# Kernel optimization log

Hardware: AMD Instinct MI355X
Metric: run time of the kernel (lower is better)

## Reference

```python
import jax, jax.numpy as jnp
import numpy as np

B = 16384
D = 128
N_LAYER = 2
USER_NUM, ITEM_NUM, ENTITY_NUM = 100000, 50000, 50000
H1, H2 = 256, 128  # hidden_layers


def setup_inputs() -> dict:
    key = jax.random.key(0)
    ks = jax.random.split(key, 20)
    inp = {
        'user_ids': jax.random.randint(ks[0], (B,), 0, USER_NUM),
        'item_ids': jax.random.randint(ks[1], (B,), 0, ITEM_NUM),
        'rec_target': jax.random.uniform(ks[2], (B,), dtype=jnp.float32),
        # embedding tables
        'user_tbl': jax.random.normal(ks[3], (USER_NUM, D), dtype=jnp.float32) * 0.02,
        'item_tbl': jax.random.normal(ks[4], (ITEM_NUM, D), dtype=jnp.float32) * 0.02,
        'entity_tbl': jax.random.normal(ks[5], (ENTITY_NUM, D), dtype=jnp.float32) * 0.02,
        # cross-compress weights (torch.rand -> uniform)
        'w_vv': jax.random.uniform(ks[6], (D, 1), dtype=jnp.float32),
        'w_ev': jax.random.uniform(ks[7], (D, 1), dtype=jnp.float32),
        'w_ve': jax.random.uniform(ks[8], (D, 1), dtype=jnp.float32),
        'w_ee': jax.random.uniform(ks[9], (D, 1), dtype=jnp.float32),
        'bias_v': jax.random.uniform(ks[10], (1,), dtype=jnp.float32),
        'bias_e': jax.random.uniform(ks[11], (1,), dtype=jnp.float32),
        # user low MLP (Linear D->D)
        'Wu': jax.random.normal(ks[12], (D, D), dtype=jnp.float32) * 0.05,
        'bu': jnp.zeros((D,), dtype=jnp.float32),
        # rec MLP: 2D -> H1 -> H2 -> 1
        'W1': jax.random.normal(ks[13], (2 * D, H1), dtype=jnp.float32) * 0.05,
        'b1': jnp.zeros((H1,), dtype=jnp.float32),
        'W2': jax.random.normal(ks[14], (H1, H2), dtype=jnp.float32) * 0.05,
        'b2': jnp.zeros((H2,), dtype=jnp.float32),
        'W3': jax.random.normal(ks[15], (H2, 1), dtype=jnp.float32) * 0.05,
        'b3': jnp.zeros((1,), dtype=jnp.float32),
    }
    return inp


def _cross_compress(item, head, w_vv, w_ev, w_ve, w_ee, bias_v, bias_e):
    # c[b,i,j] = item[b,i]*head[b,j]; c_t[b,i,j] = head[b,i]*item[b,j]
    # (c @ w)[b,i] = item[b,i] * (head @ w)[b]; (c_t @ w)[b,i] = head[b,i] * (item @ w)[b]
    hv = head @ w_vv  # [B,1]
    iv = item @ w_ev  # [B,1]
    he = head @ w_ve  # [B,1]
    ie = item @ w_ee  # [B,1]
    item_c = item * hv + head * iv + bias_v
    head_c = item * he + head * ie + bias_e
    return item_c, head_c


def reference(user_ids, item_ids, rec_target, user_tbl, item_tbl, entity_tbl,
              w_vv, w_ev, w_ve, w_ee, bias_v, bias_e,
              Wu, bu, W1, b1, W2, b2, W3, b3):
    # train_type == 'rec' branch
    user_embed = user_tbl[user_ids]      # [B, D]
    item_embed = item_tbl[item_ids]      # [B, D]
    head_embed = entity_tbl[item_ids]    # [B, D]
    for _ in range(N_LAYER):
        user_embed = jax.nn.relu(user_embed @ Wu + bu)  # linear_layer (dropout=identity at eval)
        item_embed, head_embed = _cross_compress(
            item_embed, head_embed, w_vv, w_ev, w_ve, w_ee, bias_v, bias_e)
    high = jnp.concatenate([user_embed, item_embed], axis=1)  # [B, 2D]
    h = jax.nn.relu(high @ W1 + b1)
    h = jax.nn.relu(h @ W2 + b2)
    rec_out = jax.nn.relu(h @ W3 + b3)  # [B, 1]
    return rec_out[:, 0], rec_target
```

## Files before the change

### kernel.cpp

```cpp
#include <hip/hip_runtime.h>

#define BATCH 16384
#define DIM 128

typedef __attribute__((ext_vector_type(8))) short short8;
typedef __attribute__((ext_vector_type(4))) float floatx4;

__device__ __forceinline__ ushort f2bf(float f) {
    union { float f; uint u; } c; c.f = f;
    return (ushort)((c.u + 0x7FFFu + ((c.u >> 16) & 1u)) >> 16);
}
__device__ __forceinline__ float bf2f(ushort h) {
    union { uint u; float f; } c; c.u = ((uint)h) << 16;
    return c.f;
}
__device__ __forceinline__ ushort4 f4_to_bf4(float4 v) {
    return make_ushort4(f2bf(v.x), f2bf(v.y), f2bf(v.z), f2bf(v.w));
}

__device__ __forceinline__ int slot_idx(int KT, int m, int k) {
    return (((m >> 4) * KT + (k >> 5)) << 6) + (((k >> 3) & 3) << 4) + (m & 15);
}

__global__ __launch_bounds__(256) void convert_kernel(
    const float* __restrict__ Wu, const float* __restrict__ W1,
    const float* __restrict__ W2, short8* __restrict__ WF)
{
    const int f    = blockIdx.x * 4 + (threadIdx.x >> 6);
    const int lane = threadIdx.x & 63;
    const int q = lane >> 4, r = lane & 15;
    const float* W; int N, nt, kf, fl; short8* dst;
    if (f < 32)       { W = Wu; N = 128; fl = f;       nt = fl >> 2; kf = fl & 3; dst = WF;         }
    else if (f < 160) { W = W1; N = 256; fl = f - 32;  nt = fl >> 3; kf = fl & 7; dst = WF + 2048;  }
    else              { W = W2; N = 128; fl = f - 160; nt = fl >> 3; kf = fl & 7; dst = WF + 10240; }
    const int n = nt * 16 + r, k0 = kf * 32 + q * 8;
    short8 v;
    #pragma unroll
    for (int j = 0; j < 8; ++j)
        v[j] = (short)f2bf(W[(size_t)(k0 + j) * N + n]);
    dst[fl * 64 + lane] = v;
}

template<int KF, int NT, int DKT>
__device__ __forceinline__ void layer_mfma(
    const short8* __restrict__ src, const short8* __restrict__ WF,
    const float* __restrict__ bias, ushort* __restrict__ dst, int tid)
{
    const int wave = tid >> 6, lane = tid & 63;
    const int q = lane >> 4, r = lane & 15;
    short8 a[2][KF];
    #pragma unroll
    for (int mt = 0; mt < 2; ++mt)
        #pragma unroll
        for (int kf = 0; kf < KF; ++kf)
            a[mt][kf] = src[(mt * KF + kf) * 64 + lane];
    #pragma unroll
    for (int nt = wave; nt < NT; nt += 4) {
        const int col = nt * 16 + r;
        short8 b[KF];
        #pragma unroll
        for (int kf = 0; kf < KF; ++kf)
            b[kf] = WF[(nt * KF + kf) * 64 + lane];
        const float bs = bias[col];
        const int kc = col >> 5, qc = (col >> 3) & 3, e = col & 7;
        #pragma unroll
        for (int mt = 0; mt < 2; ++mt) {
            floatx4 acc = {0.f, 0.f, 0.f, 0.f};
            #pragma unroll
            for (int kf = 0; kf < KF; ++kf)
                acc = __builtin_amdgcn_mfma_f32_16x16x32_bf16(a[mt][kf], b[kf], acc, 0, 0, 0);
            #pragma unroll
            for (int rr = 0; rr < 4; ++rr) {
                const int rlow = q * 4 + rr;
                dst[(size_t)((((mt * DKT + kc) << 6) + (qc << 4) + rlow) * 8 + e)] =
                    f2bf(fmaxf(acc[rr] + bs, 0.f));
            }
        }
    }
}

__global__ __launch_bounds__(256) void fused_kernel(
    const int* __restrict__ user_ids, const int* __restrict__ item_ids,
    const float* __restrict__ rec_target,
    const float* __restrict__ user_tbl, const float* __restrict__ item_tbl,
    const float* __restrict__ entity_tbl,
    const float* __restrict__ w_vv, const float* __restrict__ w_ev,
    const float* __restrict__ w_ve, const float* __restrict__ w_ee,
    const float* __restrict__ bias_v, const float* __restrict__ bias_e,
    const short8* __restrict__ WF, const float* __restrict__ bu,
    const float* __restrict__ b1, const float* __restrict__ b2,
    const float* __restrict__ W3, const float* __restrict__ b3,
    float* __restrict__ out)
{
    __shared__ short8 sU0[512];
    __shared__ short8 sU1[512];
    __shared__ short8 sHI[1024];
    __shared__ short8 sH1[1024];
    __shared__ short8 sH2[512];

    const int r0   = blockIdx.x * 32;
    const int tid  = threadIdx.x;
    const int wave = tid >> 6, lane = tid & 63;
    const int q    = lane >> 4, r = lane & 15;
    const int row  = tid >> 3, l = tid & 7;

    short8 bw[2][4];
    #pragma unroll
    for (int i = 0; i < 2; ++i) {
        const int nt = wave + i * 4;
        #pragma unroll
        for (int kf = 0; kf < 4; ++kf)
            bw[i][kf] = WF[(nt * 4 + kf) * 64 + lane];
    }

    if (tid < 32) out[BATCH + r0 + tid] = rec_target[r0 + tid];

    {
        const int uid = user_ids[r0 + row];
        const float4* src = (const float4*)(user_tbl + (size_t)uid * DIM + l * 16);
        ushort* p = (ushort*)sU0;
        #pragma unroll
        for (int i = 0; i < 4; ++i) {
            const int col = l * 16 + i * 4;
            *(ushort4*)&p[slot_idx(4, row, col) * 8 + (col & 7)] = f4_to_bf4(src[i]);
        }
    }

    {
        const int id = item_ids[r0 + row];
        const float4* ip = (const float4*)(item_tbl   + (size_t)id * DIM + l * 16);
        const float4* hp = (const float4*)(entity_tbl + (size_t)id * DIM + l * 16);
        float4 it4[4], hd4[4];
        #pragma unroll
        for (int i = 0; i < 4; ++i) { it4[i] = ip[i]; hd4[i] = hp[i]; }
        const float bv = bias_v[0], be = bias_e[0];
        #pragma unroll
        for (int lay = 0; lay < 2; ++lay) {
            float hv = 0.f, iv = 0.f, he = 0.f, ie = 0.f;
            #pragma unroll
            for (int i = 0; i < 4; ++i) {
                float4 wvv = ((const float4*)w_vv)[l * 4 + i];
                float4 wev = ((const float4*)w_ev)[l * 4 + i];
                float4 wve = ((const float4*)w_ve)[l * 4 + i];
                float4 wee = ((const float4*)w_ee)[l * 4 + i];
                hv += hd4[i].x * wvv.x + hd4[i].y * wvv.y + hd4[i].z * wvv.z + hd4[i].w * wvv.w;
                iv += it4[i].x * wev.x + it4[i].y * wev.y + it4[i].z * wev.z + it4[i].w * wev.w;
                he += hd4[i].x * wve.x + hd4[i].y * wve.y + hd4[i].z * wve.z + hd4[i].w * wve.w;
                ie += it4[i].x * wee.x + it4[i].y * wee.y + it4[i].z * wee.z + it4[i].w * wee.w;
            }
            hv += __shfl_xor(hv, 1); hv += __shfl_xor(hv, 2); hv += __shfl_xor(hv, 4);
            iv += __shfl_xor(iv, 1); iv += __shfl_xor(iv, 2); iv += __shfl_xor(iv, 4);
            he += __shfl_xor(he, 1); he += __shfl_xor(he, 2); he += __shfl_xor(he, 4);
            ie += __shfl_xor(ie, 1); ie += __shfl_xor(ie, 2); ie += __shfl_xor(ie, 4);
            #pragma unroll
            for (int i = 0; i < 4; ++i) {
                float4 t = it4[i], h = hd4[i];
                it4[i].x = t.x * hv + h.x * iv + bv;  hd4[i].x = t.x * he + h.x * ie + be;
                it4[i].y = t.y * hv + h.y * iv + bv;  hd4[i].y = t.y * he + h.y * ie + be;
                it4[i].z = t.z * hv + h.z * iv + bv;  hd4[i].z = t.z * he + h.z * ie + be;
                it4[i].w = t.w * hv + h.w * iv + bv;  hd4[i].w = t.w * he + h.w * ie + be;
            }
        }
        ushort* p = (ushort*)sHI;
        #pragma unroll
        for (int i = 0; i < 4; ++i) {
            const int col = 128 + l * 16 + i * 4;
            *(ushort4*)&p[slot_idx(8, row, col) * 8 + (col & 7)] = f4_to_bf4(it4[i]);
        }
    }
    __syncthreads();

    {
        short8 a[2][4];
        #pragma unroll
        for (int mt = 0; mt < 2; ++mt)
            #pragma unroll
            for (int kf = 0; kf < 4; ++kf)
                a[mt][kf] = sU0[(mt * 4 + kf) * 64 + lane];
        #pragma unroll
        for (int i = 0; i < 2; ++i) {
            const int col = (wave + i * 4) * 16 + r;
            const float bs = bu[col];
            const int kc = col >> 5, qc = (col >> 3) & 3, e = col & 7;
            #pragma unroll
            for (int mt = 0; mt < 2; ++mt) {
                floatx4 acc = {0.f, 0.f, 0.f, 0.f};
                #pragma unroll
                for (int kf = 0; kf < 4; ++kf)
                    acc = __builtin_amdgcn_mfma_f32_16x16x32_bf16(a[mt][kf], bw[i][kf], acc, 0, 0, 0);
                ushort* dst = (ushort*)sU1;
                #pragma unroll
                for (int rr = 0; rr < 4; ++rr)
                    dst[(((mt * 4 + kc) << 6) + (qc << 4) + q * 4 + rr) * 8 + e] =
                        f2bf(fmaxf(acc[rr] + bs, 0.f));
            }
        }
    }
    __syncthreads();

    {
        short8 a[2][4];
        #pragma unroll
        for (int mt = 0; mt < 2; ++mt)
            #pragma unroll
            for (int kf = 0; kf < 4; ++kf)
                a[mt][kf] = sU1[(mt * 4 + kf) * 64 + lane];
        #pragma unroll
        for (int i = 0; i < 2; ++i) {
            const int col = (wave + i * 4) * 16 + r;
            const float bs = bu[col];
            const int kc = col >> 5, qc = (col >> 3) & 3, e = col & 7;
            #pragma unroll
            for (int mt = 0; mt < 2; ++mt) {
                floatx4 acc = {0.f, 0.f, 0.f, 0.f};
                #pragma unroll
                for (int kf = 0; kf < 4; ++kf)
                    acc = __builtin_amdgcn_mfma_f32_16x16x32_bf16(a[mt][kf], bw[i][kf], acc, 0, 0, 0);
                ushort* dst = (ushort*)sHI;
                #pragma unroll
                for (int rr = 0; rr < 4; ++rr)
                    dst[(((mt * 8 + kc) << 6) + (qc << 4) + q * 4 + rr) * 8 + e] =
                        f2bf(fmaxf(acc[rr] + bs, 0.f));
            }
        }
    }
    __syncthreads();

    layer_mfma<8, 16, 8>(sHI, WF + 2048,  b1, (ushort*)sH1, tid);
    __syncthreads();
    layer_mfma<8, 8, 4>(sH1, WF + 10240,  b2, (ushort*)sH2, tid);
    __syncthreads();

    {
        float p = 0.f;
        #pragma unroll
        for (int i = 0; i < 2; ++i) {
            const int c8 = l * 2 + i;
            short8 h = sH2[(((row >> 4) * 4 + (c8 >> 2)) << 6) + ((c8 & 3) << 4) + (row & 15)];
            float4 w0 = ((const float4*)W3)[c8 * 2];
            float4 w1 = ((const float4*)W3)[c8 * 2 + 1];
            p += bf2f((ushort)h[0]) * w0.x + bf2f((ushort)h[1]) * w0.y
               + bf2f((ushort)h[2]) * w0.z + bf2f((ushort)h[3]) * w0.w
               + bf2f((ushort)h[4]) * w1.x + bf2f((ushort)h[5]) * w1.y
               + bf2f((ushort)h[6]) * w1.z + bf2f((ushort)h[7]) * w1.w;
        }
        p += __shfl_xor(p, 1); p += __shfl_xor(p, 2); p += __shfl_xor(p, 4);
        if (l == 0) out[r0 + row] = fmaxf(p + b3[0], 0.f);
    }
}

extern "C" void kernel_launch(void* const* d_in, const int* in_sizes, int n_in,
                              void* d_out, int out_size, void* d_ws, size_t ws_size,
                              hipStream_t stream)
{
    const int*   user_ids   = (const int*)  d_in[0];
    const int*   item_ids   = (const int*)  d_in[1];
    const float* rec_target = (const float*)d_in[2];
    const float* user_tbl   = (const float*)d_in[3];
    const float* item_tbl   = (const float*)d_in[4];
    const float* entity_tbl = (const float*)d_in[5];
    const float* w_vv       = (const float*)d_in[6];
    const float* w_ev       = (const float*)d_in[7];
    const float* w_ve       = (const float*)d_in[8];
    const float* w_ee       = (const float*)d_in[9];
    const float* bias_v     = (const float*)d_in[10];
    const float* bias_e     = (const float*)d_in[11];
    const float* Wu         = (const float*)d_in[12];
    const float* bu         = (const float*)d_in[13];
    const float* W1         = (const float*)d_in[14];
    const float* b1         = (const float*)d_in[15];
    const float* W2         = (const float*)d_in[16];
    const float* b2         = (const float*)d_in[17];
    const float* W3         = (const float*)d_in[18];
    const float* b3         = (const float*)d_in[19];
    float* out = (float*)d_out;

    short8* WF = (short8*)d_ws;

    convert_kernel<<<56, 256, 0, stream>>>(Wu, W1, W2, WF);
    fused_kernel<<<BATCH / 32, 256, 0, stream>>>(
        user_ids, item_ids, rec_target, user_tbl, item_tbl, entity_tbl,
        w_vv, w_ev, w_ve, w_ee, bias_v, bias_e,
        WF, bu, b1, b2, W3, b3, out);
}
```

Baseline: 155.6 us.

## Use 512-thread blocks, hoist gathers, fuse final W3 dot into layer-2 epilogue

The fused kernel now runs 8 waves per 32-row block instead of 4, so each wave owns one output column tile in the 128-wide layers and two in the 256-wide layer. All three embedding gathers are issued up front, and the cross-compress math now runs while the first user MLP layer is computed. The final H2->1 projection is folded into the second MLP layer's epilogue using shuffle reductions and a small shared partial-sum array, which removes the sH2 buffer and one LDS round trip. In exchange, each wave reloads the A fragments per m-tile, and the larger blocks may change occupancy and register pressure.

```diff
diff --git a/kernel.cpp b/kernel.cpp
--- a/kernel.cpp
+++ b/kernel.cpp
@@ -9,13 +9,6 @@
 __device__ __forceinline__ ushort f2bf(float f) {
     union { float f; uint u; } c; c.f = f;
     return (ushort)((c.u + 0x7FFFu + ((c.u >> 16) & 1u)) >> 16);
-}
-__device__ __forceinline__ float bf2f(ushort h) {
-    union { uint u; float f; } c; c.u = ((uint)h) << 16;
-    return c.f;
-}
-__device__ __forceinline__ ushort4 f4_to_bf4(float4 v) {
-    return make_ushort4(f2bf(v.x), f2bf(v.y), f2bf(v.z), f2bf(v.w));
 }
 
 __device__ __forceinline__ int slot_idx(int KT, int m, int k) {
@@ -41,45 +34,7 @@
     dst[fl * 64 + lane] = v;
 }
 
-template<int KF, int NT, int DKT>
-__device__ __forceinline__ void layer_mfma(
-    const short8* __restrict__ src, const short8* __restrict__ WF,
-    const float* __restrict__ bias, ushort* __restrict__ dst, int tid)
-{
-    const int wave = tid >> 6, lane = tid & 63;
-    const int q = lane >> 4, r = lane & 15;
-    short8 a[2][KF];
-    #pragma unroll
-    for (int mt = 0; mt < 2; ++mt)
-        #pragma unroll
-        for (int kf = 0; kf < KF; ++kf)
-            a[mt][kf] = src[(mt * KF + kf) * 64 + lane];
-    #pragma unroll
-    for (int nt = wave; nt < NT; nt += 4) {
-        const int col = nt * 16 + r;
-        short8 b[KF];
-        #pragma unroll
-        for (int kf = 0; kf < KF; ++kf)
-            b[kf] = WF[(nt * KF + kf) * 64 + lane];
-        const float bs = bias[col];
-        const int kc = col >> 5, qc = (col >> 3) & 3, e = col & 7;
-        #pragma unroll
-        for (int mt = 0; mt < 2; ++mt) {
-            floatx4 acc = {0.f, 0.f, 0.f, 0.f};
-            #pragma unroll
-            for (int kf = 0; kf < KF; ++kf)
-                acc = __builtin_amdgcn_mfma_f32_16x16x32_bf16(a[mt][kf], b[kf], acc, 0, 0, 0);
-            #pragma unroll
-            for (int rr = 0; rr < 4; ++rr) {
-                const int rlow = q * 4 + rr;
-                dst[(size_t)((((mt * DKT + kc) << 6) + (qc << 4) + rlow) * 8 + e)] =
-                    f2bf(fmaxf(acc[rr] + bs, 0.f));
-            }
-        }
-    }
-}
-
-__global__ __launch_bounds__(256) void fused_kernel(
+__global__ __launch_bounds__(512) void fused_kernel(
     const int* __restrict__ user_ids, const int* __restrict__ item_ids,
     const float* __restrict__ rec_target,
     const float* __restrict__ user_tbl, const float* __restrict__ item_tbl,
@@ -96,64 +51,84 @@
     __shared__ short8 sU1[512];
     __shared__ short8 sHI[1024];
     __shared__ short8 sH1[1024];
-    __shared__ short8 sH2[512];
+    __shared__ float  sP[8][32];
 
     const int r0   = blockIdx.x * 32;
     const int tid  = threadIdx.x;
     const int wave = tid >> 6, lane = tid & 63;
     const int q    = lane >> 4, r = lane & 15;
-    const int row  = tid >> 3, l = tid & 7;
-
-    short8 bw[2][4];
+    const int row  = tid >> 4, l = tid & 15;
+
+    const int uid = user_ids[r0 + row];
+    const int iid = item_ids[r0 + row];
+    const float4* up = (const float4*)(user_tbl   + (size_t)uid * DIM + l * 8);
+    const float4* ip = (const float4*)(item_tbl   + (size_t)iid * DIM + l * 8);
+    const float4* hp = (const float4*)(entity_tbl + (size_t)iid * DIM + l * 8);
+    float4 us4[2] = { up[0], up[1] };
+    float4 it4[2] = { ip[0], ip[1] };
+    float4 hd4[2] = { hp[0], hp[1] };
+
+    short8 bw[4];
     #pragma unroll
-    for (int i = 0; i < 2; ++i) {
-        const int nt = wave + i * 4;
-        #pragma unroll
-        for (int kf = 0; kf < 4; ++kf)
-            bw[i][kf] = WF[(nt * 4 + kf) * 64 + lane];
-    }
+    for (int kf = 0; kf < 4; ++kf)
+        bw[kf] = WF[(wave * 4 + kf) * 64 + lane];
 
     if (tid < 32) out[BATCH + r0 + tid] = rec_target[r0 + tid];
 
     {
-        const int uid = user_ids[r0 + row];
-        const float4* src = (const float4*)(user_tbl + (size_t)uid * DIM + l * 16);
-        ushort* p = (ushort*)sU0;
-        #pragma unroll
-        for (int i = 0; i < 4; ++i) {
-            const int col = l * 16 + i * 4;
-            *(ushort4*)&p[slot_idx(4, row, col) * 8 + (col & 7)] = f4_to_bf4(src[i]);
-        }
-    }
-
-    {
-        const int id = item_ids[r0 + row];
-        const float4* ip = (const float4*)(item_tbl   + (size_t)id * DIM + l * 16);
-        const float4* hp = (const float4*)(entity_tbl + (size_t)id * DIM + l * 16);
-        float4 it4[4], hd4[4];
-        #pragma unroll
-        for (int i = 0; i < 4; ++i) { it4[i] = ip[i]; hd4[i] = hp[i]; }
+        const float* uf = (const float*)us4;
+        short8 v;
+        #pragma unroll
+        for (int j = 0; j < 8; ++j) v[j] = (short)f2bf(uf[j]);
+        sU0[slot_idx(4, row, l * 8)] = v;
+    }
+    __syncthreads();
+
+    {
+        short8 a[2][4];
+        #pragma unroll
+        for (int mt = 0; mt < 2; ++mt)
+            #pragma unroll
+            for (int kf = 0; kf < 4; ++kf)
+                a[mt][kf] = sU0[(mt * 4 + kf) * 64 + lane];
+        const int col = wave * 16 + r;
+        const float bs = bu[col];
+        const int kc = col >> 5, qc = (col >> 3) & 3, e = col & 7;
+        ushort* dst = (ushort*)sU1;
+        #pragma unroll
+        for (int mt = 0; mt < 2; ++mt) {
+            floatx4 acc = {0.f, 0.f, 0.f, 0.f};
+            #pragma unroll
+            for (int kf = 0; kf < 4; ++kf)
+                acc = __builtin_amdgcn_mfma_f32_16x16x32_bf16(a[mt][kf], bw[kf], acc, 0, 0, 0);
+            #pragma unroll
+            for (int rr = 0; rr < 4; ++rr)
+                dst[(((mt * 4 + kc) << 6) + (qc << 4) + q * 4 + rr) * 8 + e] =
+                    f2bf(fmaxf(acc[rr] + bs, 0.f));
+        }
+    }
+    {
         const float bv = bias_v[0], be = bias_e[0];
         #pragma unroll
         for (int lay = 0; lay < 2; ++lay) {
             float hv = 0.f, iv = 0.f, he = 0.f, ie = 0.f;
             #pragma unroll
-            for (int i = 0; i < 4; ++i) {
-                float4 wvv = ((const float4*)w_vv)[l * 4 + i];
-                float4 wev = ((const float4*)w_ev)[l * 4 + i];
-                float4 wve = ((const float4*)w_ve)[l * 4 + i];
-                float4 wee = ((const float4*)w_ee)[l * 4 + i];
+            for (int i = 0; i < 2; ++i) {
+                float4 wvv = ((const float4*)w_vv)[l * 2 + i];
+                float4 wev = ((const float4*)w_ev)[l * 2 + i];
+                float4 wve = ((const float4*)w_ve)[l * 2 + i];
+                float4 wee = ((const float4*)w_ee)[l * 2 + i];
                 hv += hd4[i].x * wvv.x + hd4[i].y * wvv.y + hd4[i].z * wvv.z + hd4[i].w * wvv.w;
                 iv += it4[i].x * wev.x + it4[i].y * wev.y + it4[i].z * wev.z + it4[i].w * wev.w;
                 he += hd4[i].x * wve.x + hd4[i].y * wve.y + hd4[i].z * wve.z + hd4[i].w * wve.w;
                 ie += it4[i].x * wee.x + it4[i].y * wee.y + it4[i].z * wee.z + it4[i].w * wee.w;
             }
-            hv += __shfl_xor(hv, 1); hv += __shfl_xor(hv, 2); hv += __shfl_xor(hv, 4);
-            iv += __shfl_xor(iv, 1); iv += __shfl_xor(iv, 2); iv += __shfl_xor(iv, 4);
-            he += __shfl_xor(he, 1); he += __shfl_xor(he, 2); he += __shfl_xor(he, 4);
-            ie += __shfl_xor(ie, 1); ie += __shfl_xor(ie, 2); ie += __shfl_xor(ie, 4);
-            #pragma unroll
-            for (int i = 0; i < 4; ++i) {
+            hv += __shfl_xor(hv, 1); hv += __shfl_xor(hv, 2); hv += __shfl_xor(hv, 4); hv += __shfl_xor(hv, 8);
+            iv += __shfl_xor(iv, 1); iv += __shfl_xor(iv, 2); iv += __shfl_xor(iv, 4); iv += __shfl_xor(iv, 8);
+            he += __shfl_xor(he, 1); he += __shfl_xor(he, 2); he += __shfl_xor(he, 4); he += __shfl_xor(he, 8);
+            ie += __shfl_xor(ie, 1); ie += __shfl_xor(ie, 2); ie += __shfl_xor(ie, 4); ie += __shfl_xor(ie, 8);
+            #pragma unroll
+            for (int i = 0; i < 2; ++i) {
                 float4 t = it4[i], h = hd4[i];
                 it4[i].x = t.x * hv + h.x * iv + bv;  hd4[i].x = t.x * he + h.x * ie + be;
                 it4[i].y = t.y * hv + h.y * iv + bv;  hd4[i].y = t.y * he + h.y * ie + be;
@@ -161,12 +136,11 @@
                 it4[i].w = t.w * hv + h.w * iv + bv;  hd4[i].w = t.w * he + h.w * ie + be;
             }
         }
-        ushort* p = (ushort*)sHI;
-        #pragma unroll
-        for (int i = 0; i < 4; ++i) {
-            const int col = 128 + l * 16 + i * 4;
-            *(ushort4*)&p[slot_idx(8, row, col) * 8 + (col & 7)] = f4_to_bf4(it4[i]);
-        }
+        const float* itf = (const float*)it4;
+        short8 v;
+        #pragma unroll
+        for (int j = 0; j < 8; ++j) v[j] = (short)f2bf(itf[j]);
+        sHI[slot_idx(8, row, 128 + l * 8)] = v;
     }
     __syncthreads();
 
@@ -176,47 +150,48 @@
         for (int mt = 0; mt < 2; ++mt)
             #pragma unroll
             for (int kf = 0; kf < 4; ++kf)
-                a[mt][kf] = sU0[(mt * 4 + kf) * 64 + lane];
-        #pragma unroll
-        for (int i = 0; i < 2; ++i) {
-            const int col = (wave + i * 4) * 16 + r;
-            const float bs = bu[col];
-            const int kc = col >> 5, qc = (col >> 3) & 3, e = col & 7;
-            #pragma unroll
-            for (int mt = 0; mt < 2; ++mt) {
+                a[mt][kf] = sU1[(mt * 4 + kf) * 64 + lane];
+        const int col = wave * 16 + r;
+        const float bs = bu[col];
+        const int kc = col >> 5, qc = (col >> 3) & 3, e = col & 7;
+        ushort* dst = (ushort*)sHI;
+        #pragma unroll
+        for (int mt = 0; mt < 2; ++mt) {
+            floatx4 acc = {0.f, 0.f, 0.f, 0.f};
+            #pragma unroll
+            for (int kf = 0; kf < 4; ++kf)
+                acc = __builtin_amdgcn_mfma_f32_16x16x32_bf16(a[mt][kf], bw[kf], acc, 0, 0, 0);
+            #pragma unroll
+            for (int rr = 0; rr < 4; ++rr)
+                dst[(((mt * 8 + kc) << 6) + (qc << 4) + q * 4 + rr) * 8 + e] =
+                    f2bf(fmaxf(acc[rr] + bs, 0.f));
+        }
+    }
+    __syncthreads();
+
+    {
+        const short8* WF1 = WF + 2048;
+        ushort* dst = (ushort*)sH1;
+        #pragma unroll
+        for (int mt = 0; mt < 2; ++mt) {
+            short8 a[8];
+            #pragma unroll
+            for (int kf = 0; kf < 8; ++kf)
+                a[kf] = sHI[(mt * 8 + kf) * 64 + lane];
+            #pragma unroll
+            for (int i = 0; i < 2; ++i) {
+                const int nt = wave + i * 8;
+                short8 b[8];
+                #pragma unroll
+                for (int kf = 0; kf < 8; ++kf)
+                    b[kf] = WF1[(nt * 8 + kf) * 64 + lane];
+                const int col = nt * 16 + r;
+                const float bs = b1[col];
+                const int kc = col >> 5, qc = (col >> 3) & 3, e = col & 7;
                 floatx4 acc = {0.f, 0.f, 0.f, 0.f};
                 #pragma unroll
-                for (int kf = 0; kf < 4; ++kf)
-                    acc = __builtin_amdgcn_mfma_f32_16x16x32_bf16(a[mt][kf], bw[i][kf], acc, 0, 0, 0);
-                ushort* dst = (ushort*)sU1;
-                #pragma unroll
-                for (int rr = 0; rr < 4; ++rr)
-                    dst[(((mt * 4 + kc) << 6) + (qc << 4) + q * 4 + rr) * 8 + e] =
-                        f2bf(fmaxf(acc[rr] + bs, 0.f));
-            }
-        }
-    }
-    __syncthreads();
-
-    {
-        short8 a[2][4];
-        #pragma unroll
-        for (int mt = 0; mt < 2; ++mt)
-            #pragma unroll
-            for (int kf = 0; kf < 4; ++kf)
-                a[mt][kf] = sU1[(mt * 4 + kf) * 64 + lane];
-        #pragma unroll
-        for (int i = 0; i < 2; ++i) {
-            const int col = (wave + i * 4) * 16 + r;
-            const float bs = bu[col];
-            const int kc = col >> 5, qc = (col >> 3) & 3, e = col & 7;
-            #pragma unroll
-            for (int mt = 0; mt < 2; ++mt) {
-                floatx4 acc = {0.f, 0.f, 0.f, 0.f};
-                #pragma unroll
-                for (int kf = 0; kf < 4; ++kf)
-                    acc = __builtin_amdgcn_mfma_f32_16x16x32_bf16(a[mt][kf], bw[i][kf], acc, 0, 0, 0);
-                ushort* dst = (ushort*)sHI;
+                for (int kf = 0; kf < 8; ++kf)
+                    acc = __builtin_amdgcn_mfma_f32_16x16x32_bf16(a[kf], b[kf], acc, 0, 0, 0);
                 #pragma unroll
                 for (int rr = 0; rr < 4; ++rr)
                     dst[(((mt * 8 + kc) << 6) + (qc << 4) + q * 4 + rr) * 8 + e] =
@@ -226,26 +201,54 @@
     }
     __syncthreads();
 
-    layer_mfma<8, 16, 8>(sHI, WF + 2048,  b1, (ushort*)sH1, tid);
-    __syncthreads();
-    layer_mfma<8, 8, 4>(sH1, WF + 10240,  b2, (ushort*)sH2, tid);
-    __syncthreads();
-
-    {
+    {
+        const short8* WF2 = WF + 10240;
+        const int col = wave * 16 + r;
+        const float bs  = b2[col];
+        const float w3c = W3[col];
+        short8 b[8];
+        #pragma unroll
+        for (int kf = 0; kf < 8; ++kf)
+            b[kf] = WF2[(wave * 8 + kf) * 64 + lane];
+        float v[2][4];
+        #pragma unroll
+        for (int mt = 0; mt < 2; ++mt) {
+            short8 a[8];
+            #pragma unroll
+            for (int kf = 0; kf < 8; ++kf)
+                a[kf] = sH1[(mt * 8 + kf) * 64 + lane];
+            floatx4 acc = {0.f, 0.f, 0.f, 0.f};
+            #pragma unroll
+            for (int kf = 0; kf < 8; ++kf)
+                acc = __builtin_amdgcn_mfma_f32_16x16x32_bf16(a[kf], b[kf], acc, 0, 0, 0);
+            #pragma unroll
+            for (int rr = 0; rr < 4; ++rr)
+                v[mt][rr] = fmaxf(acc[rr] + bs, 0.f) * w3c;
+        }
+        #pragma unroll
+        for (int mt = 0; mt < 2; ++mt)
+            #pragma unroll
+            for (int rr = 0; rr < 4; ++rr) {
+                float t = v[mt][rr];
+                t += __shfl_xor(t, 1); t += __shfl_xor(t, 2);
+                t += __shfl_xor(t, 4); t += __shfl_xor(t, 8);
+                v[mt][rr] = t;
+            }
+        if (r == 0) {
+            #pragma unroll
+            for (int mt = 0; mt < 2; ++mt)
+                #pragma unroll
+                for (int rr = 0; rr < 4; ++rr)
+                    sP[wave][mt * 16 + q * 4 + rr] = v[mt][rr];
+        }
+    }
+    __syncthreads();
+
+    if (tid < 32) {
         float p = 0.f;
         #pragma unroll
-        for (int i = 0; i < 2; ++i) {
-            const int c8 = l * 2 + i;
-            short8 h = sH2[(((row >> 4) * 4 + (c8 >> 2)) << 6) + ((c8 & 3) << 4) + (row & 15)];
-            float4 w0 = ((const float4*)W3)[c8 * 2];
-            float4 w1 = ((const float4*)W3)[c8 * 2 + 1];
-            p += bf2f((ushort)h[0]) * w0.x + bf2f((ushort)h[1]) * w0.y
-               + bf2f((ushort)h[2]) * w0.z + bf2f((ushort)h[3]) * w0.w
-               + bf2f((ushort)h[4]) * w1.x + bf2f((ushort)h[5]) * w1.y
-               + bf2f((ushort)h[6]) * w1.z + bf2f((ushort)h[7]) * w1.w;
-        }
-        p += __shfl_xor(p, 1); p += __shfl_xor(p, 2); p += __shfl_xor(p, 4);
-        if (l == 0) out[r0 + row] = fmaxf(p + b3[0], 0.f);
+        for (int w = 0; w < 8; ++w) p += sP[w][tid];
+        out[r0 + tid] = fmaxf(p + b3[0], 0.f);
     }
 }
 
@@ -278,7 +281,7 @@
     short8* WF = (short8*)d_ws;
 
     convert_kernel<<<56, 256, 0, stream>>>(Wu, W1, W2, WF);
-    fused_kernel<<<BATCH / 32, 256, 0, stream>>>(
+    fused_kernel<<<BATCH / 32, 512, 0, stream>>>(
         user_ids, item_ids, rec_target, user_tbl, item_tbl, entity_tbl,
         w_vv, w_ev, w_ve, w_ee, bias_v, bias_e,
         WF, bu, b1, b2, W3, b3, out);
```

After: 158.2 us. No clear change (+1.7%).
